# Kernel tuning notes

Hardware: AMD Instinct MI355X
Metric: run time of the kernel (lower is better)

The kernel has to match this reference:

```python
import jax, jax.numpy as jnp
import numpy as np

B, T, E, H = 4, 1024, 768, 12
D = E // H          # head_dim = 64
TEMP = 1.0          # temperature t


def setup_inputs() -> dict:
    key = jax.random.key(0)
    ks = jax.random.split(key, 19)
    inp = {}
    for i, name in enumerate(["query1", "query2", "query3", "key", "value"]):
        inp[name] = jax.random.normal(ks[i], (B, T, E), dtype=jnp.float32)
    # learned params: 6 Linear(E, E) layers (q1,q2,q3,k,v,out), torch layout W:[out,in]
    names = ["q1", "q2", "q3", "k", "v", "o"]
    for j, n in enumerate(names):
        inp[f"W{n}"] = jax.random.normal(ks[5 + 2 * j], (E, E), dtype=jnp.float32) * 0.02
        inp[f"b{n}"] = jax.random.normal(ks[6 + 2 * j], (E,), dtype=jnp.float32) * 0.02
    return inp


def _heads(x):
    # [B,T,E] -> [B,T,H,D]
    return x.reshape(B, T, H, D)


def _flat_softmax_scores(q, k):
    # q,k: [B,T,H,D]; scores: [B,H,T,T]
    s = jnp.einsum("bthd,bshd->bhts", q, k) / jnp.sqrt(jnp.float32(D))
    # global softmax over flattened T*T per (B,H), then scale by T
    s = jax.nn.softmax((s / TEMP).reshape(B, H, T * T), axis=-1)
    return s.reshape(B, H, T, T) * T


def reference(query1, query2, query3, key, value,
              Wq1, bq1, Wq2, bq2, Wq3, bq3, Wk, bk, Wv, bv, Wo, bo):
    q1 = _heads(query1 @ Wq1.T + bq1)
    q2 = _heads(query2 @ Wq2.T + bq2)
    q3 = _heads(query3 @ Wq3.T + bq3)
    k = _heads(key @ Wk.T + bk)
    v = _heads(value @ Wv.T + bv)
    a1 = _flat_softmax_scores(q1, k)
    a2 = _flat_softmax_scores(q2, k)
    a3 = _flat_softmax_scores(q3, k)
    attn = (a1 + a2 + a3) / 3.0          # [B,H,T,T]
    out = jnp.einsum("bhts,bshd->bthd", attn, v).reshape(B, T, E)
    return out @ Wo.T + bo
```

## Files before the change

kernel.cpp:

```cpp
#include <hip/hip_runtime.h>
#include <hip/hip_bf16.h>

#define Bb 4
#define Tt 1024
#define Ee 768
#define Hh 12
#define Dd 64
#define NTOK (Bb*Tt)

#define QSCALE 0.18033688f

typedef __attribute__((ext_vector_type(8))) short bf16x8;
typedef __attribute__((ext_vector_type(4))) float f32x4;

__device__ __forceinline__ f32x4 mfma16(bf16x8 a, bf16x8 b, f32x4 c) {
  return __builtin_amdgcn_mfma_f32_16x16x32_bf16(a, b, c, 0, 0, 0);
}
__device__ __forceinline__ float exp2x(float x) {
  return __builtin_amdgcn_exp2f(x);
}

__device__ __forceinline__ ushort f2b(float f) {
  uint u = __builtin_bit_cast(uint, f);
  return (ushort)((u + 0x7fffu + ((u >> 16) & 1u)) >> 16);
}
__device__ __forceinline__ uint pack2(float a, float b) {
  return (uint)f2b(a) | ((uint)f2b(b) << 16);
}

typedef const __attribute__((address_space(1))) void GV;
typedef __attribute__((address_space(3))) void LV;
__device__ __forceinline__ void gload16(const void* g, void* l) {
  __builtin_amdgcn_global_load_lds((GV*)g, (LV*)l, 16, 0, 0);
}

struct CvtSeg { const float* src; ushort* dst; int n8; float scale; };
struct CvtArgs { CvtSeg seg[11]; };

__global__ __launch_bounds__(256) void convert_kernel(CvtArgs a) {
  const CvtSeg s = a.seg[blockIdx.y];
  const int i = blockIdx.x * 256 + threadIdx.x;
  if (i >= s.n8) return;
  const float4 v0 = ((const float4*)s.src)[2*i];
  const float4 v1 = ((const float4*)s.src)[2*i + 1];
  uint4 o;
  o.x = pack2(v0.x * s.scale, v0.y * s.scale);
  o.y = pack2(v0.z * s.scale, v0.w * s.scale);
  o.z = pack2(v1.x * s.scale, v1.y * s.scale);
  o.w = pack2(v1.z * s.scale, v1.w * s.scale);
  ((uint4*)s.dst)[i] = o;
}

template<bool OUT_BF16>
__device__ __forceinline__ void gemm_bf16(
    const ushort* __restrict__ A, const ushort* __restrict__ Bw,
    const float* __restrict__ bias, const float bscale, void* __restrict__ Cp,
    const int K, const int N)
{
  __shared__ ushort Ash[128][64];
  __shared__ ushort Bsh[128][64];
  const int tid  = threadIdx.x;
  const int lane = tid & 63;
  const int wave = tid >> 6;
  const int m0 = blockIdx.x * 128;
  const int n0 = blockIdx.y * 128;
  const int wm = (wave >> 1) << 6;
  const int wn = (wave & 1) << 6;
  const int srow = lane >> 3;
  const int scol = ((lane & 7) ^ srow) << 3;
  const ushort* Ag = A  + (size_t)(m0 + wave*8 + srow) * K + scol;
  const ushort* Bg = Bw + (size_t)(n0 + wave*8 + srow) * K + scol;

  f32x4 acc[4][4] = {};
  for (int k0 = 0; k0 < K; k0 += 64) {
    __syncthreads();
#pragma unroll
    for (int rr = 0; rr < 4; rr++) {
      gload16(Ag + (size_t)(rr*32) * K + k0, &Ash[rr*32 + wave*8][0]);
      gload16(Bg + (size_t)(rr*32) * K + k0, &Bsh[rr*32 + wave*8][0]);
    }
    __syncthreads();
#pragma unroll
    for (int kk = 0; kk < 2; kk++) {
      const int pcb = (((lane >> 4) << 4) + kk*64) ^ ((lane & 7) << 4);
      bf16x8 af[4], bfv[4];
#pragma unroll
      for (int m = 0; m < 4; m++)
        af[m] = *(const bf16x8*)((const char*)&Ash[wm + m*16 + (lane & 15)][0] + pcb);
#pragma unroll
      for (int n = 0; n < 4; n++)
        bfv[n] = *(const bf16x8*)((const char*)&Bsh[wn + n*16 + (lane & 15)][0] + pcb);
#pragma unroll
      for (int m = 0; m < 4; m++)
#pragma unroll
        for (int n = 0; n < 4; n++)
          acc[m][n] = mfma16(af[m], bfv[n], acc[m][n]);
    }
  }
#pragma unroll
  for (int n = 0; n < 4; n++) {
    const int col = n0 + wn + n*16 + (lane & 15);
    const float bv = bias[col] * bscale;
#pragma unroll
    for (int m = 0; m < 4; m++) {
#pragma unroll
      for (int r = 0; r < 4; r++) {
        const int row = m0 + wm + m*16 + ((lane >> 4) << 2) + r;
        const float v = acc[m][n][r] + bv;
        if (OUT_BF16) ((ushort*)Cp)[(size_t)row * N + col] = f2b(v);
        else          ((float*)Cp)[(size_t)row * N + col] = v;
      }
    }
  }
}

struct ProjPtrs {
  const ushort* X[5];
  const ushort* W[5];
  const float* b[5];
  float bscale[5];
  ushort* out[5];
};

__global__ __launch_bounds__(256, 2) void proj5_kernel(ProjPtrs p) {
  const int z = blockIdx.z;
  gemm_bf16<true>(p.X[z], p.W[z], p.b[z], p.bscale[z], p.out[z], Ee, Ee);
}

__global__ __launch_bounds__(256, 2) void outproj_kernel(
    const ushort* __restrict__ A, const ushort* __restrict__ W,
    const float* __restrict__ bias, float* __restrict__ C) {
  gemm_bf16<false>(A, W, bias, 1.0f, C, Ee, Ee);
}


__global__ __launch_bounds__(256, 4) void attn_pass1(
    const ushort* __restrict__ q1, const ushort* __restrict__ q2,
    const ushort* __restrict__ q3, const ushort* __restrict__ kmat,
    float* __restrict__ Z)
{
  const int bh = blockIdx.x;
  const int b = bh / Hh, h = bh % Hh;
  const int lane = threadIdx.x & 63;
  const int wave = threadIdx.x >> 6;
  const int trow0 = blockIdx.y * 64 + wave * 16;

  __shared__ ushort Ksh[64][64];

  const int srow = lane >> 3;
  const int scolb = ((lane & 7) ^ srow) << 4;
  const ushort* Kg = kmat + (size_t)(b*Tt)*Ee + h*Dd;

  const ushort* qs[3] = {q1, q2, q3};
  bf16x8 qf[3][2];
#pragma unroll
  for (int j = 0; j < 3; j++)
#pragma unroll
    for (int kk = 0; kk < 2; kk++) {
      const int t = trow0 + (lane & 15);
      const int d = kk*32 + ((lane >> 4) << 3);
      qf[j][kk] = *(const bf16x8*)(qs[j] + ((size_t)(b*Tt + t))*Ee + h*Dd + d);
    }

  float zacc[3] = {0.f, 0.f, 0.f};
  for (int s0 = 0; s0 < Tt; s0 += 64) {
    __syncthreads();
#pragma unroll
    for (int rr = 0; rr < 2; rr++) {
      const int rowbase = rr*32 + wave*8;
      gload16((const char*)(Kg + (size_t)(s0 + rowbase + srow)*Ee) + scolb,
              &Ksh[rowbase][0]);
    }
    __syncthreads();
    bf16x8 kf[4][2];
#pragma unroll
    for (int n = 0; n < 4; n++)
#pragma unroll
      for (int kk = 0; kk < 2; kk++)
        kf[n][kk] = *(const bf16x8*)((const char*)&Ksh[n*16 + (lane & 15)][0] +
                      ((((lane >> 4) << 4) + kk*64) ^ ((lane & 7) << 4)));
#pragma unroll
    for (int j = 0; j < 3; j++) {
      f32x4 sacc[4] = {};
#pragma unroll
      for (int kk = 0; kk < 2; kk++)
#pragma unroll
        for (int n = 0; n < 4; n++)
          sacc[n] = mfma16(qf[j][kk], kf[n][kk], sacc[n]);
      float s = 0.f;
#pragma unroll
      for (int n = 0; n < 4; n++)
#pragma unroll
        for (int r = 0; r < 4; r++)
          s += exp2x(sacc[n][r]);
      zacc[j] += s;
    }
  }
#pragma unroll
  for (int j = 0; j < 3; j++) {
    float v = zacc[j];
#pragma unroll
    for (int off = 32; off > 0; off >>= 1) v += __shfl_xor(v, off, 64);
    if (lane == 0) atomicAdd(&Z[bh*3 + j], v);
  }
}

__global__ __launch_bounds__(256, 3) void attn_pass2(
    const ushort* __restrict__ q1, const ushort* __restrict__ q2,
    const ushort* __restrict__ q3, const ushort* __restrict__ kmat,
    const ushort* __restrict__ vmat, const float* __restrict__ Z,
    ushort* __restrict__ O)
{
  const int bh = blockIdx.x;
  const int b = bh / Hh, h = bh % Hh;
  const int lane = threadIdx.x & 63;
  const int wave = threadIdx.x >> 6;
  const int trow0 = blockIdx.y * 64 + wave * 16;

  __shared__ ushort Ksh[64][64];
  __shared__ ushort Vsh[64][72];
  __shared__ ushort Psh[64][72];

  const int srow = lane >> 3;
  const int scolb = ((lane & 7) ^ srow) << 4;
  const ushort* Kg = kmat + (size_t)(b*Tt)*Ee + h*Dd;

  const ushort* qs[3] = {q1, q2, q3};
  bf16x8 qf[3][2];
#pragma unroll
  for (int j = 0; j < 3; j++)
#pragma unroll
    for (int kk = 0; kk < 2; kk++) {
      const int t = trow0 + (lane & 15);
      const int d = kk*32 + ((lane >> 4) << 3);
      qf[j][kk] = *(const bf16x8*)(qs[j] + ((size_t)(b*Tt + t))*Ee + h*Dd + d);
    }

  float cj[3];
#pragma unroll
  for (int j = 0; j < 3; j++) cj[j] = (float)Tt / (3.0f * Z[bh*3 + j]);

  f32x4 oacc[4] = {};

  for (int s0 = 0; s0 < Tt; s0 += 64) {
    __syncthreads();
#pragma unroll
    for (int rr = 0; rr < 2; rr++) {
      const int rowbase = rr*32 + wave*8;
      gload16((const char*)(Kg + (size_t)(s0 + rowbase + srow)*Ee) + scolb,
              &Ksh[rowbase][0]);
    }
    for (int i = threadIdx.x; i < 512; i += 256) {
      const int r = i & 63;
      const int c = (i >> 6) << 3;
      bf16x8 v = *(const bf16x8*)(vmat + ((size_t)(b*Tt + s0 + r))*Ee + h*Dd + c);
#pragma unroll
      for (int u = 0; u < 8; u++) Vsh[c + u][r] = (ushort)v[u];
    }
    __syncthreads();
    bf16x8 kf[4][2];
#pragma unroll
    for (int n = 0; n < 4; n++)
#pragma unroll
      for (int kk = 0; kk < 2; kk++)
        kf[n][kk] = *(const bf16x8*)((const char*)&Ksh[n*16 + (lane & 15)][0] +
                      ((((lane >> 4) << 4) + kk*64) ^ ((lane & 7) << 4)));

    f32x4 pacc[4] = {};
#pragma unroll
    for (int j = 0; j < 3; j++) {
      f32x4 sacc[4] = {};
#pragma unroll
      for (int kk = 0; kk < 2; kk++)
#pragma unroll
        for (int n = 0; n < 4; n++)
          sacc[n] = mfma16(qf[j][kk], kf[n][kk], sacc[n]);
#pragma unroll
      for (int n = 0; n < 4; n++)
#pragma unroll
        for (int r = 0; r < 4; r++)
          pacc[n][r] += cj[j] * exp2x(sacc[n][r]);
    }
#pragma unroll
    for (int n = 0; n < 4; n++)
#pragma unroll
      for (int r = 0; r < 4; r++)
        Psh[wave*16 + ((lane >> 4) << 2) + r][n*16 + (lane & 15)] = f2b(pacc[n][r]);
#pragma unroll
    for (int kk = 0; kk < 2; kk++) {
      bf16x8 pa, vb[4];
      pa = *(const bf16x8*)&Psh[wave*16 + (lane & 15)][kk*32 + ((lane >> 4) << 3)];
#pragma unroll
      for (int n = 0; n < 4; n++)
        vb[n] = *(const bf16x8*)&Vsh[n*16 + (lane & 15)][kk*32 + ((lane >> 4) << 3)];
#pragma unroll
      for (int n = 0; n < 4; n++)
        oacc[n] = mfma16(pa, vb[n], oacc[n]);
    }
  }
#pragma unroll
  for (int n = 0; n < 4; n++)
#pragma unroll
    for (int r = 0; r < 4; r++) {
      const int t = trow0 + ((lane >> 4) << 2) + r;
      const int d = n*16 + (lane & 15);
      O[((size_t)(b*Tt + t))*Ee + h*Dd + d] = f2b(oacc[n][r]);
    }
}

extern "C" void kernel_launch(void* const* d_in, const int* in_sizes, int n_in,
                              void* d_out, int out_size, void* d_ws, size_t ws_size,
                              hipStream_t stream) {
  const float* X[5];
  for (int i = 0; i < 5; i++) X[i] = (const float*)d_in[i];
  const float* W[6];  const float* bias[6];
  for (int j = 0; j < 6; j++) {
    W[j]    = (const float*)d_in[5 + 2*j];
    bias[j] = (const float*)d_in[6 + 2*j];
  }

  char* ws = (char*)d_ws;
  const size_t segX = (size_t)NTOK * Ee * sizeof(ushort);
  const size_t segW = (size_t)Ee * Ee * sizeof(ushort);
  ushort* Xbf[5];
  for (int i = 0; i < 5; i++) Xbf[i] = (ushort*)(ws + i*segX);
  ushort* Wbf[6];
  for (int j = 0; j < 6; j++) Wbf[j] = (ushort*)(ws + 5*segX + j*segW);
  ushort* Pout[5];
  for (int i = 0; i < 5; i++) Pout[i] = (ushort*)(ws + 5*segX + 6*segW + i*segX);
  ushort* Ob = Xbf[0];
  float*  Zp = (float*)(ws + 10*segX + 6*segW);

  CvtArgs ca;
  for (int i = 0; i < 5; i++) ca.seg[i]     = {X[i], Xbf[i], NTOK*Ee/8, 1.0f};
  for (int j = 0; j < 6; j++) ca.seg[5 + j] = {W[j], Wbf[j], Ee*Ee/8,
                                               (j < 3) ? QSCALE : 1.0f};

  ProjPtrs pp;
  for (int i = 0; i < 5; i++) {
    pp.X[i] = Xbf[i]; pp.W[i] = Wbf[i]; pp.b[i] = bias[i]; pp.out[i] = Pout[i];
    pp.bscale[i] = (i < 3) ? QSCALE : 1.0f;
  }

  hipMemsetAsync(Zp, 0, 48*3*sizeof(float), stream);
  convert_kernel<<<dim3(1536, 11), 256, 0, stream>>>(ca);
  proj5_kernel<<<dim3(32, 6, 5), 256, 0, stream>>>(pp);
  attn_pass1<<<dim3(48, 16), 256, 0, stream>>>(Pout[0], Pout[1], Pout[2], Pout[3], Zp);
  attn_pass2<<<dim3(48, 16), 256, 0, stream>>>(Pout[0], Pout[1], Pout[2], Pout[3], Pout[4], Zp, Ob);
  outproj_kernel<<<dim3(32, 6), 256, 0, stream>>>(Ob, Wbf[5], bias[5], (float*)d_out);
}
```

Baseline: 162.6 us.

## Fuse attention passes into one pass with per-query unnormalized outputs and a combine kernel

Pass 1 (the softmax-denominator pass) and pass 2 (the weighted-sum pass) are merged into a single kernel. It computes QK^T and exp once per tile and accumulates both the per-query normalizers Z and three unnormalized exp(S)·V outputs. Those outputs are written in place over the q buffers. A small elementwise combine kernel then applies the Tt/(3·Z_j) scales and sums the three outputs before the output projection. This removes the second QK^T and exp computation and a K reload. The cost is three times the PV MFMA work, a larger register footprint, and extra global traffic for the three intermediate outputs.

```diff
diff --git a/kernel.cpp b/kernel.cpp
--- a/kernel.cpp
+++ b/kernel.cpp
@@ -26,6 +26,9 @@
 }
 __device__ __forceinline__ uint pack2(float a, float b) {
   return (uint)f2b(a) | ((uint)f2b(b) << 16);
+}
+__device__ __forceinline__ float b2f(ushort u) {
+  return __builtin_bit_cast(float, (uint)u << 16);
 }
 
 typedef const __attribute__((address_space(1))) void GV;
@@ -133,10 +136,9 @@
   gemm_bf16<false>(A, W, bias, 1.0f, C, Ee, Ee);
 }
 
-
-__global__ __launch_bounds__(256, 4) void attn_pass1(
-    const ushort* __restrict__ q1, const ushort* __restrict__ q2,
-    const ushort* __restrict__ q3, const ushort* __restrict__ kmat,
+__global__ __launch_bounds__(256, 3) void attn_fused(
+    ushort* qu1, ushort* qu2, ushort* qu3,
+    const ushort* __restrict__ kmat, const ushort* __restrict__ vmat,
     float* __restrict__ Z)
 {
   const int bh = blockIdx.x;
@@ -146,12 +148,14 @@
   const int trow0 = blockIdx.y * 64 + wave * 16;
 
   __shared__ ushort Ksh[64][64];
+  __shared__ ushort Vsh[64][72];
+  __shared__ ushort Psh[64][72];
 
   const int srow = lane >> 3;
   const int scolb = ((lane & 7) ^ srow) << 4;
   const ushort* Kg = kmat + (size_t)(b*Tt)*Ee + h*Dd;
 
-  const ushort* qs[3] = {q1, q2, q3};
+  ushort* qs[3] = {qu1, qu2, qu3};
   bf16x8 qf[3][2];
 #pragma unroll
   for (int j = 0; j < 3; j++)
@@ -163,6 +167,8 @@
     }
 
   float zacc[3] = {0.f, 0.f, 0.f};
+  f32x4 uacc[3][4] = {};
+
   for (int s0 = 0; s0 < Tt; s0 += 64) {
     __syncthreads();
 #pragma unroll
@@ -171,85 +177,6 @@
       gload16((const char*)(Kg + (size_t)(s0 + rowbase + srow)*Ee) + scolb,
               &Ksh[rowbase][0]);
     }
-    __syncthreads();
-    bf16x8 kf[4][2];
-#pragma unroll
-    for (int n = 0; n < 4; n++)
-#pragma unroll
-      for (int kk = 0; kk < 2; kk++)
-        kf[n][kk] = *(const bf16x8*)((const char*)&Ksh[n*16 + (lane & 15)][0] +
-                      ((((lane >> 4) << 4) + kk*64) ^ ((lane & 7) << 4)));
-#pragma unroll
-    for (int j = 0; j < 3; j++) {
-      f32x4 sacc[4] = {};
-#pragma unroll
-      for (int kk = 0; kk < 2; kk++)
-#pragma unroll
-        for (int n = 0; n < 4; n++)
-          sacc[n] = mfma16(qf[j][kk], kf[n][kk], sacc[n]);
-      float s = 0.f;
-#pragma unroll
-      for (int n = 0; n < 4; n++)
-#pragma unroll
-        for (int r = 0; r < 4; r++)
-          s += exp2x(sacc[n][r]);
-      zacc[j] += s;
-    }
-  }
-#pragma unroll
-  for (int j = 0; j < 3; j++) {
-    float v = zacc[j];
-#pragma unroll
-    for (int off = 32; off > 0; off >>= 1) v += __shfl_xor(v, off, 64);
-    if (lane == 0) atomicAdd(&Z[bh*3 + j], v);
-  }
-}
-
-__global__ __launch_bounds__(256, 3) void attn_pass2(
-    const ushort* __restrict__ q1, const ushort* __restrict__ q2,
-    const ushort* __restrict__ q3, const ushort* __restrict__ kmat,
-    const ushort* __restrict__ vmat, const float* __restrict__ Z,
-    ushort* __restrict__ O)
-{
-  const int bh = blockIdx.x;
-  const int b = bh / Hh, h = bh % Hh;
-  const int lane = threadIdx.x & 63;
-  const int wave = threadIdx.x >> 6;
-  const int trow0 = blockIdx.y * 64 + wave * 16;
-
-  __shared__ ushort Ksh[64][64];
-  __shared__ ushort Vsh[64][72];
-  __shared__ ushort Psh[64][72];
-
-  const int srow = lane >> 3;
-  const int scolb = ((lane & 7) ^ srow) << 4;
-  const ushort* Kg = kmat + (size_t)(b*Tt)*Ee + h*Dd;
-
-  const ushort* qs[3] = {q1, q2, q3};
-  bf16x8 qf[3][2];
-#pragma unroll
-  for (int j = 0; j < 3; j++)
-#pragma unroll
-    for (int kk = 0; kk < 2; kk++) {
-      const int t = trow0 + (lane & 15);
-      const int d = kk*32 + ((lane >> 4) << 3);
-      qf[j][kk] = *(const bf16x8*)(qs[j] + ((size_t)(b*Tt + t))*Ee + h*Dd + d);
-    }
-
-  float cj[3];
-#pragma unroll
-  for (int j = 0; j < 3; j++) cj[j] = (float)Tt / (3.0f * Z[bh*3 + j]);
-
-  f32x4 oacc[4] = {};
-
-  for (int s0 = 0; s0 < Tt; s0 += 64) {
-    __syncthreads();
-#pragma unroll
-    for (int rr = 0; rr < 2; rr++) {
-      const int rowbase = rr*32 + wave*8;
-      gload16((const char*)(Kg + (size_t)(s0 + rowbase + srow)*Ee) + scolb,
-              &Ksh[rowbase][0]);
-    }
     for (int i = threadIdx.x; i < 512; i += 256) {
       const int r = i & 63;
       const int c = (i >> 6) << 3;
@@ -258,54 +185,96 @@
       for (int u = 0; u < 8; u++) Vsh[c + u][r] = (ushort)v[u];
     }
     __syncthreads();
-    bf16x8 kf[4][2];
+
+    f32x4 sacc[3][4] = {};
+#pragma unroll
+    for (int kk = 0; kk < 2; kk++) {
+      bf16x8 kf[4];
+#pragma unroll
+      for (int n = 0; n < 4; n++)
+        kf[n] = *(const bf16x8*)((const char*)&Ksh[n*16 + (lane & 15)][0] +
+                  ((((lane >> 4) << 4) + kk*64) ^ ((lane & 7) << 4)));
+#pragma unroll
+      for (int j = 0; j < 3; j++)
+#pragma unroll
+        for (int n = 0; n < 4; n++)
+          sacc[j][n] = mfma16(kf[n], qf[j][kk], sacc[j][n]);
+    }
+
+    bf16x8 vb[2][4];
+#pragma unroll
+    for (int kk = 0; kk < 2; kk++)
+#pragma unroll
+      for (int n = 0; n < 4; n++)
+        vb[kk][n] = *(const bf16x8*)&Vsh[n*16 + (lane & 15)][kk*32 + ((lane >> 4) << 3)];
+
+    const int prow = wave*16 + (lane & 15);
+#pragma unroll
+    for (int j = 0; j < 3; j++) {
+      float zl = 0.f;
+#pragma unroll
+      for (int n = 0; n < 4; n++) {
+        const float e0 = exp2x(sacc[j][n][0]);
+        const float e1 = exp2x(sacc[j][n][1]);
+        const float e2 = exp2x(sacc[j][n][2]);
+        const float e3 = exp2x(sacc[j][n][3]);
+        zl += (e0 + e1) + (e2 + e3);
+        *(uint2*)&Psh[prow][n*16 + ((lane >> 4) << 2)] =
+            make_uint2(pack2(e0, e1), pack2(e2, e3));
+      }
+      zacc[j] += zl;
+#pragma unroll
+      for (int kk = 0; kk < 2; kk++) {
+        const bf16x8 pa = *(const bf16x8*)&Psh[wave*16 + (lane & 15)]
+                                              [kk*32 + ((lane >> 4) << 3)];
+#pragma unroll
+        for (int n = 0; n < 4; n++)
+          uacc[j][n] = mfma16(pa, vb[kk][n], uacc[j][n]);
+      }
+    }
+  }
+
+#pragma unroll
+  for (int j = 0; j < 3; j++)
 #pragma unroll
     for (int n = 0; n < 4; n++)
 #pragma unroll
-      for (int kk = 0; kk < 2; kk++)
-        kf[n][kk] = *(const bf16x8*)((const char*)&Ksh[n*16 + (lane & 15)][0] +
-                      ((((lane >> 4) << 4) + kk*64) ^ ((lane & 7) << 4)));
-
-    f32x4 pacc[4] = {};
-#pragma unroll
-    for (int j = 0; j < 3; j++) {
-      f32x4 sacc[4] = {};
-#pragma unroll
-      for (int kk = 0; kk < 2; kk++)
-#pragma unroll
-        for (int n = 0; n < 4; n++)
-          sacc[n] = mfma16(qf[j][kk], kf[n][kk], sacc[n]);
-#pragma unroll
-      for (int n = 0; n < 4; n++)
-#pragma unroll
-        for (int r = 0; r < 4; r++)
-          pacc[n][r] += cj[j] * exp2x(sacc[n][r]);
-    }
-#pragma unroll
-    for (int n = 0; n < 4; n++)
-#pragma unroll
-      for (int r = 0; r < 4; r++)
-        Psh[wave*16 + ((lane >> 4) << 2) + r][n*16 + (lane & 15)] = f2b(pacc[n][r]);
-#pragma unroll
-    for (int kk = 0; kk < 2; kk++) {
-      bf16x8 pa, vb[4];
-      pa = *(const bf16x8*)&Psh[wave*16 + (lane & 15)][kk*32 + ((lane >> 4) << 3)];
-#pragma unroll
-      for (int n = 0; n < 4; n++)
-        vb[n] = *(const bf16x8*)&Vsh[n*16 + (lane & 15)][kk*32 + ((lane >> 4) << 3)];
-#pragma unroll
-      for (int n = 0; n < 4; n++)
-        oacc[n] = mfma16(pa, vb[n], oacc[n]);
-    }
-  }
-#pragma unroll
-  for (int n = 0; n < 4; n++)
-#pragma unroll
-    for (int r = 0; r < 4; r++) {
-      const int t = trow0 + ((lane >> 4) << 2) + r;
-      const int d = n*16 + (lane & 15);
-      O[((size_t)(b*Tt + t))*Ee + h*Dd + d] = f2b(oacc[n][r]);
-    }
+      for (int r = 0; r < 4; r++) {
+        const int t = trow0 + ((lane >> 4) << 2) + r;
+        const int d = n*16 + (lane & 15);
+        qs[j][((size_t)(b*Tt + t))*Ee + h*Dd + d] = f2b(uacc[j][n][r]);
+      }
+#pragma unroll
+  for (int j = 0; j < 3; j++) {
+    float v = zacc[j];
+#pragma unroll
+    for (int off = 32; off > 0; off >>= 1) v += __shfl_xor(v, off, 64);
+    if (lane == 0) atomicAdd(&Z[bh*3 + j], v);
+  }
+}
+
+__global__ __launch_bounds__(256) void combine_kernel(
+    const ushort* __restrict__ U1, const ushort* __restrict__ U2,
+    const ushort* __restrict__ U3, const float* __restrict__ Z,
+    ushort* __restrict__ O)
+{
+  const int i = blockIdx.x * 256 + threadIdx.x;
+  const int e4 = i << 2;
+  const int ecol = e4 % Ee;
+  const int b = e4 / (Ee * Tt);
+  const int bh3 = (b * Hh + ecol / Dd) * 3;
+  const float c1 = (float)Tt / (3.0f * Z[bh3 + 0]);
+  const float c2 = (float)Tt / (3.0f * Z[bh3 + 1]);
+  const float c3 = (float)Tt / (3.0f * Z[bh3 + 2]);
+  const ushort4 u1 = *(const ushort4*)(U1 + e4);
+  const ushort4 u2 = *(const ushort4*)(U2 + e4);
+  const ushort4 u3 = *(const ushort4*)(U3 + e4);
+  ushort4 o;
+  o.x = f2b(c1*b2f(u1.x) + c2*b2f(u2.x) + c3*b2f(u3.x));
+  o.y = f2b(c1*b2f(u1.y) + c2*b2f(u2.y) + c3*b2f(u3.y));
+  o.z = f2b(c1*b2f(u1.z) + c2*b2f(u2.z) + c3*b2f(u3.z));
+  o.w = f2b(c1*b2f(u1.w) + c2*b2f(u2.w) + c3*b2f(u3.w));
+  *(ushort4*)(O + e4) = o;
 }
 
 extern "C" void kernel_launch(void* const* d_in, const int* in_sizes, int n_in,
@@ -345,7 +314,9 @@
   hipMemsetAsync(Zp, 0, 48*3*sizeof(float), stream);
   convert_kernel<<<dim3(1536, 11), 256, 0, stream>>>(ca);
   proj5_kernel<<<dim3(32, 6, 5), 256, 0, stream>>>(pp);
-  attn_pass1<<<dim3(48, 16), 256, 0, stream>>>(Pout[0], Pout[1], Pout[2], Pout[3], Zp);
-  attn_pass2<<<dim3(48, 16), 256, 0, stream>>>(Pout[0], Pout[1], Pout[2], Pout[3], Pout[4], Zp, Ob);
+  attn_fused<<<dim3(48, 16), 256, 0, stream>>>(Pout[0], Pout[1], Pout[2],
+                                               Pout[3], Pout[4], Zp);
+  combine_kernel<<<dim3((NTOK*Ee/4)/256), 256, 0, stream>>>(
+      Pout[0], Pout[1], Pout[2], Zp, Ob);
   outproj_kernel<<<dim3(32, 6), 256, 0, stream>>>(Ob, Wbf[5], bias[5], (float*)d_out);
 }
```

Result: slower. 165.9 us (+2.1%).

## Double-buffer LDS in GEMM and attention passes, split pass1 over key halves

Applied to the files above, without the earlier changes.

The projection GEMM and both attention passes now use two LDS buffers, so the next K/V (or A/B) tile is fetched while the current one is consumed, with one barrier per iteration instead of two. Pass1 splits the key range across a new grid z dimension and raises its occupancy hint. Pass2 stages V through registers and transposes it into LDS only after compute. It also computes S transposed so each lane can write P to LDS as packed 64-bit stores. The cost is twice the LDS per block and more register pressure, which may lower occupancy.

```diff
diff --git a/kernel.cpp b/kernel.cpp
--- a/kernel.cpp
+++ b/kernel.cpp
@@ -57,8 +57,8 @@
     const float* __restrict__ bias, const float bscale, void* __restrict__ Cp,
     const int K, const int N)
 {
-  __shared__ ushort Ash[128][64];
-  __shared__ ushort Bsh[128][64];
+  __shared__ ushort Ash[2][128][64];
+  __shared__ ushort Bsh[2][128][64];
   const int tid  = threadIdx.x;
   const int lane = tid & 63;
   const int wave = tid >> 6;
@@ -71,31 +71,40 @@
   const ushort* Ag = A  + (size_t)(m0 + wave*8 + srow) * K + scol;
   const ushort* Bg = Bw + (size_t)(n0 + wave*8 + srow) * K + scol;
 
+  auto stage = [&](int buf, int k0) {
+#pragma unroll
+    for (int rr = 0; rr < 4; rr++) {
+      gload16(Ag + (size_t)(rr*32) * K + k0, &Ash[buf][rr*32 + wave*8][0]);
+      gload16(Bg + (size_t)(rr*32) * K + k0, &Bsh[buf][rr*32 + wave*8][0]);
+    }
+  };
+
+  stage(0, 0);
+  asm volatile("s_waitcnt vmcnt(0)" ::: "memory");
+  __syncthreads();
+
+  const int nk = K / 64;
   f32x4 acc[4][4] = {};
-  for (int k0 = 0; k0 < K; k0 += 64) {
-    __syncthreads();
-#pragma unroll
-    for (int rr = 0; rr < 4; rr++) {
-      gload16(Ag + (size_t)(rr*32) * K + k0, &Ash[rr*32 + wave*8][0]);
-      gload16(Bg + (size_t)(rr*32) * K + k0, &Bsh[rr*32 + wave*8][0]);
-    }
-    __syncthreads();
+  for (int kt = 0; kt < nk; kt++) {
+    const int cur = kt & 1;
+    if (kt + 1 < nk) stage(cur ^ 1, (kt + 1) * 64);
 #pragma unroll
     for (int kk = 0; kk < 2; kk++) {
       const int pcb = (((lane >> 4) << 4) + kk*64) ^ ((lane & 7) << 4);
       bf16x8 af[4], bfv[4];
 #pragma unroll
       for (int m = 0; m < 4; m++)
-        af[m] = *(const bf16x8*)((const char*)&Ash[wm + m*16 + (lane & 15)][0] + pcb);
-#pragma unroll
-      for (int n = 0; n < 4; n++)
-        bfv[n] = *(const bf16x8*)((const char*)&Bsh[wn + n*16 + (lane & 15)][0] + pcb);
+        af[m] = *(const bf16x8*)((const char*)&Ash[cur][wm + m*16 + (lane & 15)][0] + pcb);
+#pragma unroll
+      for (int n = 0; n < 4; n++)
+        bfv[n] = *(const bf16x8*)((const char*)&Bsh[cur][wn + n*16 + (lane & 15)][0] + pcb);
 #pragma unroll
       for (int m = 0; m < 4; m++)
 #pragma unroll
         for (int n = 0; n < 4; n++)
           acc[m][n] = mfma16(af[m], bfv[n], acc[m][n]);
     }
+    __syncthreads();
   }
 #pragma unroll
   for (int n = 0; n < 4; n++) {
@@ -134,7 +143,7 @@
 }
 
 
-__global__ __launch_bounds__(256, 4) void attn_pass1(
+__global__ __launch_bounds__(256, 6) void attn_pass1(
     const ushort* __restrict__ q1, const ushort* __restrict__ q2,
     const ushort* __restrict__ q3, const ushort* __restrict__ kmat,
     float* __restrict__ Z)
@@ -144,12 +153,22 @@
   const int lane = threadIdx.x & 63;
   const int wave = threadIdx.x >> 6;
   const int trow0 = blockIdx.y * 64 + wave * 16;
-
-  __shared__ ushort Ksh[64][64];
+  const int sbase = blockIdx.z * (Tt/2);
+
+  __shared__ ushort Ksh[2][64][64];
 
   const int srow = lane >> 3;
   const int scolb = ((lane & 7) ^ srow) << 4;
   const ushort* Kg = kmat + (size_t)(b*Tt)*Ee + h*Dd;
+
+  auto stageK = [&](int buf, int s0) {
+#pragma unroll
+    for (int rr = 0; rr < 2; rr++) {
+      const int rowbase = rr*32 + wave*8;
+      gload16((const char*)(Kg + (size_t)(s0 + rowbase + srow)*Ee) + scolb,
+              &Ksh[buf][rowbase][0]);
+    }
+  };
 
   const ushort* qs[3] = {q1, q2, q3};
   bf16x8 qf[3][2];
@@ -162,22 +181,20 @@
       qf[j][kk] = *(const bf16x8*)(qs[j] + ((size_t)(b*Tt + t))*Ee + h*Dd + d);
     }
 
+  stageK(0, sbase);
+  asm volatile("s_waitcnt vmcnt(0)" ::: "memory");
+  __syncthreads();
+
   float zacc[3] = {0.f, 0.f, 0.f};
-  for (int s0 = 0; s0 < Tt; s0 += 64) {
-    __syncthreads();
-#pragma unroll
-    for (int rr = 0; rr < 2; rr++) {
-      const int rowbase = rr*32 + wave*8;
-      gload16((const char*)(Kg + (size_t)(s0 + rowbase + srow)*Ee) + scolb,
-              &Ksh[rowbase][0]);
-    }
-    __syncthreads();
+  for (int it = 0; it < 8; it++) {
+    const int cur = it & 1;
+    if (it + 1 < 8) stageK(cur ^ 1, sbase + (it + 1) * 64);
     bf16x8 kf[4][2];
 #pragma unroll
     for (int n = 0; n < 4; n++)
 #pragma unroll
       for (int kk = 0; kk < 2; kk++)
-        kf[n][kk] = *(const bf16x8*)((const char*)&Ksh[n*16 + (lane & 15)][0] +
+        kf[n][kk] = *(const bf16x8*)((const char*)&Ksh[cur][n*16 + (lane & 15)][0] +
                       ((((lane >> 4) << 4) + kk*64) ^ ((lane & 7) << 4)));
 #pragma unroll
     for (int j = 0; j < 3; j++) {
@@ -195,6 +212,7 @@
           s += exp2x(sacc[n][r]);
       zacc[j] += s;
     }
+    __syncthreads();
   }
 #pragma unroll
   for (int j = 0; j < 3; j++) {
@@ -213,68 +231,92 @@
 {
   const int bh = blockIdx.x;
   const int b = bh / Hh, h = bh % Hh;
-  const int lane = threadIdx.x & 63;
-  const int wave = threadIdx.x >> 6;
+  const int tid  = threadIdx.x;
+  const int lane = tid & 63;
+  const int wave = tid >> 6;
+  const int g    = lane >> 4;
   const int trow0 = blockIdx.y * 64 + wave * 16;
 
-  __shared__ ushort Ksh[64][64];
-  __shared__ ushort Vsh[64][72];
+  __shared__ ushort Ksh[2][64][64];
+  __shared__ ushort Vsh[2][64][72];
   __shared__ ushort Psh[64][72];
 
   const int srow = lane >> 3;
   const int scolb = ((lane & 7) ^ srow) << 4;
   const ushort* Kg = kmat + (size_t)(b*Tt)*Ee + h*Dd;
-
-  const ushort* qs[3] = {q1, q2, q3};
-  bf16x8 qf[3][2];
-#pragma unroll
-  for (int j = 0; j < 3; j++)
-#pragma unroll
-    for (int kk = 0; kk < 2; kk++) {
-      const int t = trow0 + (lane & 15);
-      const int d = kk*32 + ((lane >> 4) << 3);
-      qf[j][kk] = *(const bf16x8*)(qs[j] + ((size_t)(b*Tt + t))*Ee + h*Dd + d);
-    }
-
-  float cj[3];
-#pragma unroll
-  for (int j = 0; j < 3; j++) cj[j] = (float)Tt / (3.0f * Z[bh*3 + j]);
-
-  f32x4 oacc[4] = {};
-
-  for (int s0 = 0; s0 < Tt; s0 += 64) {
-    __syncthreads();
+  const ushort* Vg = vmat + (size_t)(b*Tt)*Ee + h*Dd;
+
+  auto stageK = [&](int buf, int s0) {
 #pragma unroll
     for (int rr = 0; rr < 2; rr++) {
       const int rowbase = rr*32 + wave*8;
       gload16((const char*)(Kg + (size_t)(s0 + rowbase + srow)*Ee) + scolb,
-              &Ksh[rowbase][0]);
-    }
-    for (int i = threadIdx.x; i < 512; i += 256) {
-      const int r = i & 63;
-      const int c = (i >> 6) << 3;
-      bf16x8 v = *(const bf16x8*)(vmat + ((size_t)(b*Tt + s0 + r))*Ee + h*Dd + c);
-#pragma unroll
-      for (int u = 0; u < 8; u++) Vsh[c + u][r] = (ushort)v[u];
-    }
-    __syncthreads();
-    bf16x8 kf[4][2];
-#pragma unroll
-    for (int n = 0; n < 4; n++)
-#pragma unroll
-      for (int kk = 0; kk < 2; kk++)
-        kf[n][kk] = *(const bf16x8*)((const char*)&Ksh[n*16 + (lane & 15)][0] +
-                      ((((lane >> 4) << 4) + kk*64) ^ ((lane & 7) << 4)));
+              &Ksh[buf][rowbase][0]);
+    }
+  };
+
+  const int vr = tid & 63;
+  bf16x8 vstage[2];
+  auto vloadg = [&](int s0) {
+#pragma unroll
+    for (int u = 0; u < 2; u++) {
+      const int c = ((tid >> 6) + 4*u) << 3;
+      vstage[u] = *(const bf16x8*)(Vg + (size_t)(s0 + vr)*Ee + c);
+    }
+  };
+  auto vwrite = [&](int buf) {
+#pragma unroll
+    for (int u = 0; u < 2; u++) {
+      const int c = ((tid >> 6) + 4*u) << 3;
+#pragma unroll
+      for (int e = 0; e < 8; e++) Vsh[buf][c + e][vr] = (ushort)vstage[u][e];
+    }
+  };
+
+  const ushort* qs[3] = {q1, q2, q3};
+  bf16x8 qf[3][2];
+#pragma unroll
+  for (int j = 0; j < 3; j++)
+#pragma unroll
+    for (int kk = 0; kk < 2; kk++) {
+      const int t = trow0 + (lane & 15);
+      const int d = kk*32 + (g << 3);
+      qf[j][kk] = *(const bf16x8*)(qs[j] + ((size_t)(b*Tt + t))*Ee + h*Dd + d);
+    }
+
+  float cj[3];
+#pragma unroll
+  for (int j = 0; j < 3; j++) cj[j] = (float)Tt / (3.0f * Z[bh*3 + j]);
+
+  stageK(0, 0);
+  vloadg(0);
+  vwrite(0);
+  asm volatile("s_waitcnt vmcnt(0)" ::: "memory");
+  __syncthreads();
+
+  f32x4 oacc[4] = {};
+  const int prow = wave*16 + (lane & 15);
+
+  for (int it = 0; it < 16; it++) {
+    const int cur = it & 1;
+    const int s0n = (it + 1) * 64;
+    if (it + 1 < 16) { stageK(cur ^ 1, s0n); vloadg(s0n); }
 
     f32x4 pacc[4] = {};
 #pragma unroll
     for (int j = 0; j < 3; j++) {
       f32x4 sacc[4] = {};
 #pragma unroll
-      for (int kk = 0; kk < 2; kk++)
+      for (int kk = 0; kk < 2; kk++) {
+        bf16x8 kf[4];
 #pragma unroll
         for (int n = 0; n < 4; n++)
-          sacc[n] = mfma16(qf[j][kk], kf[n][kk], sacc[n]);
+          kf[n] = *(const bf16x8*)((const char*)&Ksh[cur][n*16 + (lane & 15)][0] +
+                    (((g << 4) + kk*64) ^ ((lane & 7) << 4)));
+#pragma unroll
+        for (int n = 0; n < 4; n++)
+          sacc[n] = mfma16(kf[n], qf[j][kk], sacc[n]);
+      }
 #pragma unroll
       for (int n = 0; n < 4; n++)
 #pragma unroll
@@ -283,26 +325,27 @@
     }
 #pragma unroll
     for (int n = 0; n < 4; n++)
-#pragma unroll
-      for (int r = 0; r < 4; r++)
-        Psh[wave*16 + ((lane >> 4) << 2) + r][n*16 + (lane & 15)] = f2b(pacc[n][r]);
+      *(uint2*)&Psh[prow][n*16 + (g << 2)] =
+          make_uint2(pack2(pacc[n][0], pacc[n][1]), pack2(pacc[n][2], pacc[n][3]));
 #pragma unroll
     for (int kk = 0; kk < 2; kk++) {
-      bf16x8 pa, vb[4];
-      pa = *(const bf16x8*)&Psh[wave*16 + (lane & 15)][kk*32 + ((lane >> 4) << 3)];
-#pragma unroll
-      for (int n = 0; n < 4; n++)
-        vb[n] = *(const bf16x8*)&Vsh[n*16 + (lane & 15)][kk*32 + ((lane >> 4) << 3)];
+      const bf16x8 pa = *(const bf16x8*)&Psh[wave*16 + (lane & 15)][kk*32 + (g << 3)];
+      bf16x8 vb[4];
+#pragma unroll
+      for (int n = 0; n < 4; n++)
+        vb[n] = *(const bf16x8*)&Vsh[cur][n*16 + (lane & 15)][kk*32 + (g << 3)];
 #pragma unroll
       for (int n = 0; n < 4; n++)
         oacc[n] = mfma16(pa, vb[n], oacc[n]);
     }
+    if (it + 1 < 16) vwrite(cur ^ 1);
+    __syncthreads();
   }
 #pragma unroll
   for (int n = 0; n < 4; n++)
 #pragma unroll
     for (int r = 0; r < 4; r++) {
-      const int t = trow0 + ((lane >> 4) << 2) + r;
+      const int t = trow0 + (g << 2) + r;
       const int d = n*16 + (lane & 15);
       O[((size_t)(b*Tt + t))*Ee + h*Dd + d] = f2b(oacc[n][r]);
     }
@@ -345,7 +388,7 @@
   hipMemsetAsync(Zp, 0, 48*3*sizeof(float), stream);
   convert_kernel<<<dim3(1536, 11), 256, 0, stream>>>(ca);
   proj5_kernel<<<dim3(32, 6, 5), 256, 0, stream>>>(pp);
-  attn_pass1<<<dim3(48, 16), 256, 0, stream>>>(Pout[0], Pout[1], Pout[2], Pout[3], Zp);
+  attn_pass1<<<dim3(48, 16, 2), 256, 0, stream>>>(Pout[0], Pout[1], Pout[2], Pout[3], Zp);
   attn_pass2<<<dim3(48, 16), 256, 0, stream>>>(Pout[0], Pout[1], Pout[2], Pout[3], Pout[4], Zp, Ob);
   outproj_kernel<<<dim3(32, 6), 256, 0, stream>>>(Ob, Wbf[5], bias[5], (float*)d_out);
 }
```

Result: slower. 462.8 us (+184.6%).
